# Kernel tuning notes

Measured on AMD Instinct MI355X. Metric: run time of the kernel, lower is better.

Reference implementation:

```python
import jax, jax.numpy as jnp
import numpy as np
import math

B, C, H, W, S = 8, 512, 64, 64, 4


def setup_inputs() -> dict:
    key = jax.random.key(0)
    ks = jax.random.split(key, 7)
    s = 1.0 / math.sqrt(C)  # ~ torch Linear init scale
    x = jax.random.normal(ks[0], (B, C, H, W), jnp.float32)
    Wq = jax.random.uniform(ks[1], (C, C), jnp.float32, -s, s)
    bq = jax.random.uniform(ks[2], (C,), jnp.float32, -s, s)
    Wk = jax.random.uniform(ks[3], (C, C), jnp.float32, -s, s)
    bk = jax.random.uniform(ks[4], (C,), jnp.float32, -s, s)
    Wv = jax.random.uniform(ks[5], (C, C), jnp.float32, -s, s)
    bv = jax.random.uniform(ks[6], (C,), jnp.float32, -s, s)
    return {"x": x, "Wq": Wq, "bq": bq, "Wk": Wk, "bk": bk, "Wv": Wv, "bv": bv}


def reference(x, Wq, bq, Wk, bk, Wv, bv):
    # x: (B, C, H, W). Faithful to the torch module's output, but expressed
    # in the algebraically-equivalent efficient form: the repeat_interleaved
    # attention matrix A is block-constant, so out = repeat(A_m @ Vsum).
    b, c, h, w = x.shape
    nb = (h // S) * (w // S)  # number of SxS spatial blocks
    hw = h * w
    ss = S * S

    # Block means in unfold order (bh, bw): (B, nb, C)
    x_avg = x.reshape(b, c, h // S, S, w // S, S).mean(axis=(3, 5))
    x_avg = x_avg.reshape(b, c, nb).transpose(0, 2, 1)

    Q = x_avg @ Wq.T + bq  # (B, nb, C)
    K = x_avg @ Wk.T + bk  # (B, nb, C)
    A = jax.nn.softmax(jnp.einsum('bnc,bmc->bnm', Q, K) / jnp.sqrt(jnp.float32(c)), axis=-1)

    # V over flat row-major pixels: (B, HW, C)
    x_flat = x.reshape(b, c, hw).transpose(0, 2, 1)
    V = x_flat @ Wv.T + bv

    # repeat_interleave on dim=2 means column group j of A sums V rows
    # [j*ss, (j+1)*ss) in FLAT pixel order (not spatial blocks) - faithful.
    Vsum = V.reshape(b, hw // ss, ss, c).sum(axis=2)  # (B, nb, C)
    out_small = jnp.einsum('bnm,bmc->bnc', A, Vsum)   # (B, nb, C)
    # repeat_interleave on dim=1: each block row broadcast to ss flat pixels
    out_flat = jnp.repeat(out_small, ss, axis=1)      # (B, HW, C)
    return out_flat.transpose(0, 2, 1).reshape(b, c, h, w)
```

## Files before the change

### kernel.cpp

```cpp
#include <hip/hip_runtime.h>

typedef __attribute__((ext_vector_type(8))) short short8;
typedef __attribute__((ext_vector_type(4))) float f32x4;

__device__ __forceinline__ unsigned short f2bf(float f) {
    union { float f; unsigned int i; } v; v.f = f;
    unsigned int x = v.i;
    return (unsigned short)((x + 0x7FFFu + ((x >> 16) & 1u)) >> 16);
}
__device__ __forceinline__ f32x4 mfma16(short8 a, short8 b, f32x4 c) {
    return __builtin_amdgcn_mfma_f32_16x16x32_bf16(a, b, c, 0, 0, 0);
}

__global__ void __launch_bounds__(256, 4)
prep_kernel(const float* __restrict__ x,
            const float* __restrict__ Wq,
            const float* __restrict__ Wk,
            const float* __restrict__ Wv,
            unsigned short* __restrict__ xavg,
            unsigned short* __restrict__ xsum,
            unsigned short* __restrict__ Wb)
{
    const int blk = blockIdx.x;
    const int t = threadIdx.x;
    if (blk >= 512) {
        const int f = (blk - 512) * 512 + t;
        const int m = f >> 16;
        const int o = f & 65535;
        const float4* s4 = (const float4*)((m == 0) ? Wq : (m == 1) ? Wk : Wv);
        float4 a = s4[o];
        float4 b = s4[o + 256];
        ushort4* d4 = (ushort4*)(Wb + (size_t)m * 262144);
        d4[o]       = make_ushort4(f2bf(a.x), f2bf(a.y), f2bf(a.z), f2bf(a.w));
        d4[o + 256] = make_ushort4(f2bf(b.x), f2bf(b.y), f2bf(b.z), f2bf(b.w));
        return;
    }

    const int b    = blk >> 6;
    const int rem  = blk & 63;
    const int cg   = rem >> 1;
    const int half = rem & 1;
    const int c0   = cg * 16;

    __shared__ float part[4][512];
    __shared__ unsigned short xsT[16][128];
    __shared__ unsigned short xaT[16][128];

    for (int cg4 = 0; cg4 < 4; ++cg4) {
        float4 a0, a1, b0, b1, c0v, c1, d0, d1;
        {
            const float* base = x + ((size_t)(b * 512 + c0 + cg4 * 4) * 4096) + half * 2048;
            const float4* p0 = (const float4*)(base);
            const float4* p1 = (const float4*)(base + 4096);
            const float4* p2 = (const float4*)(base + 8192);
            const float4* p3 = (const float4*)(base + 12288);
            a0 = p0[t]; a1 = p0[t + 256];
            b0 = p1[t]; b1 = p1[t + 256];
            c0v = p2[t]; c1 = p2[t + 256];
            d0 = p3[t]; d1 = p3[t + 256];
        }
        part[0][t]       = a0.x + a0.y + a0.z + a0.w;
        part[0][t + 256] = a1.x + a1.y + a1.z + a1.w;
        part[1][t]       = b0.x + b0.y + b0.z + b0.w;
        part[1][t + 256] = b1.x + b1.y + b1.z + b1.w;
        part[2][t]       = c0v.x + c0v.y + c0v.z + c0v.w;
        part[2][t + 256] = c1.x + c1.y + c1.z + c1.w;
        part[3][t]       = d0.x + d0.y + d0.z + d0.w;
        part[3][t + 256] = d1.x + d1.y + d1.z + d1.w;
        __syncthreads();

        if (t < 128) {
            const int g = t;
#pragma unroll
            for (int ci = 0; ci < 4; ++ci) {
                float4 q = *(const float4*)&part[ci][4 * g];
                xsT[cg4 * 4 + ci][g] = f2bf(q.x + q.y + q.z + q.w);
            }
        } else {
            const int n = t - 128;
            const int bh = n >> 4, bw = n & 15;
#pragma unroll
            for (int ci = 0; ci < 4; ++ci) {
                float m = (part[ci][(bh * 4 + 0) * 16 + bw] + part[ci][(bh * 4 + 1) * 16 + bw] +
                           part[ci][(bh * 4 + 2) * 16 + bw] + part[ci][(bh * 4 + 3) * 16 + bw]) * 0.0625f;
                xaT[cg4 * 4 + ci][n] = f2bf(m);
            }
        }
        __syncthreads();
    }

    {
        const int g = t >> 1, chunk = t & 1;
        const size_t rowbase = ((size_t)(b * 256) + half * 128 + g) * 512 + c0 + chunk * 8;
        short8 vs, va;
#pragma unroll
        for (int j = 0; j < 8; ++j) {
            vs[j] = (short)xsT[chunk * 8 + j][g];
            va[j] = (short)xaT[chunk * 8 + j][g];
        }
        *(short8*)(xsum + rowbase) = vs;
        *(short8*)(xavg + rowbase) = va;
    }
}

__global__ void __launch_bounds__(256, 3)
proj_gemm(const unsigned short* __restrict__ xavg,
          const unsigned short* __restrict__ xsum,
          const unsigned short* __restrict__ Wb,
          const float* __restrict__ bq,
          const float* __restrict__ bk,
          const float* __restrict__ bv,
          unsigned short* __restrict__ QK,
          unsigned short* __restrict__ VsT)
{
    const int blk = blockIdx.x;
    const int lane = threadIdx.x & 63, quad = lane >> 4, r16 = lane & 15;
    const int w = threadIdx.x >> 6;

    if (blk < 512) {
        const int wave = blk * 4 + w;
        const int mt = wave >> 5;
        const int nt = wave & 31;
        const unsigned short* xp0 = xavg + (size_t)(mt * 32 + r16) * 512 + quad * 8;
        const unsigned short* xp1 = xp0 + 16 * 512;
        const unsigned short* wp0 = Wb + (size_t)(nt * 32 + r16) * 512 + quad * 8;
        const unsigned short* wp1 = wp0 + 16 * 512;

        f32x4 a00 = {0,0,0,0}, a01 = a00, a10 = a00, a11 = a00;
#pragma unroll 4
        for (int k = 0; k < 512; k += 32) {
            short8 qa0 = *(const short8*)(xp0 + k);
            short8 qa1 = *(const short8*)(xp1 + k);
            short8 b0 = *(const short8*)(wp0 + k);
            short8 b1 = *(const short8*)(wp1 + k);
            a00 = mfma16(qa0, b0, a00); a01 = mfma16(qa0, b1, a01);
            a10 = mfma16(qa1, b0, a10); a11 = mfma16(qa1, b1, a11);
        }
        const int row0 = mt * 32 + quad * 4;
        f32x4 accs0[2] = {a00, a01};
        f32x4 accs1[2] = {a10, a11};
#pragma unroll
        for (int j = 0; j < 2; ++j) {
            const int c = nt * 32 + j * 16 + r16;
            const float bias = (c < 512) ? bq[c] : bk[c - 512];
#pragma unroll
            for (int r = 0; r < 4; ++r) {
                QK[(size_t)(row0 + r) * 1024 + c]      = f2bf(accs0[j][r] + bias);
                QK[(size_t)(row0 + 16 + r) * 1024 + c] = f2bf(accs1[j][r] + bias);
            }
        }
    } else {
        const int vblk = blk - 512;
        const int b = vblk >> 5;
        const int wib = (vblk & 31) * 4 + w;
        const int mt2 = wib >> 4;
        const int nt = wib & 15;
        const unsigned short* xp0 = xsum + (size_t)b * 131072 + (size_t)(mt2 * 32 + r16) * 512 + quad * 8;
        const unsigned short* xp1 = xp0 + 16 * 512;
        const unsigned short* wp0 = Wb + 524288 + (size_t)(nt * 32 + r16) * 512 + quad * 8;
        const unsigned short* wp1 = wp0 + 16 * 512;

        f32x4 a00 = {0,0,0,0}, a01 = a00, a10 = a00, a11 = a00;
#pragma unroll 4
        for (int k = 0; k < 512; k += 32) {
            short8 qa0 = *(const short8*)(xp0 + k);
            short8 qa1 = *(const short8*)(xp1 + k);
            short8 b0 = *(const short8*)(wp0 + k);
            short8 b1 = *(const short8*)(wp1 + k);
            a00 = mfma16(qa0, b0, a00); a01 = mfma16(qa0, b1, a01);
            a10 = mfma16(qa1, b0, a10); a11 = mfma16(qa1, b1, a11);
        }
        unsigned short* vb = VsT + (size_t)b * 131072;
        const int m0 = mt2 * 32 + quad * 4;
        f32x4 accs0[2] = {a00, a01};
        f32x4 accs1[2] = {a10, a11};
#pragma unroll
        for (int j = 0; j < 2; ++j) {
            const int c = nt * 32 + j * 16 + r16;
            const float bias = 16.f * bv[c];
#pragma unroll
            for (int r = 0; r < 4; ++r) {
                vb[(size_t)c * 256 + m0 + r]      = f2bf(accs0[j][r] + bias);
                vb[(size_t)c * 256 + m0 + 16 + r] = f2bf(accs1[j][r] + bias);
            }
        }
    }
}

__global__ void __launch_bounds__(256, 2)
score_av(const unsigned short* __restrict__ QK,
         const unsigned short* __restrict__ VsT,
         float* __restrict__ out)
{
    __shared__ union {
        float S[16][257];
        float osT[128][17];
    } u;
    __shared__ __align__(16) unsigned short Abf[16][264];

    const int b = blockIdx.y;
    const int strip = blockIdx.x >> 2;
    const int cq = blockIdx.x & 3;
    const int w = threadIdx.x >> 6, lane = threadIdx.x & 63;
    const int quad = lane >> 4, r16 = lane & 15;

    {
        const unsigned short* qp = QK + (size_t)(b * 256 + strip * 16 + r16) * 1024 + quad * 8;
        const unsigned short* kp0 = QK + (size_t)(b * 256 + w * 64 + r16) * 1024 + 512 + quad * 8;
        const unsigned short* kp1 = kp0 + 16 * 1024;
        const unsigned short* kp2 = kp0 + 32 * 1024;
        const unsigned short* kp3 = kp0 + 48 * 1024;

        f32x4 a0 = {0,0,0,0}, a1 = a0, a2 = a0, a3 = a0;
#pragma unroll 4
        for (int k = 0; k < 512; k += 32) {
            short8 qa = *(const short8*)(qp + k);
            short8 b0 = *(const short8*)(kp0 + k);
            short8 b1 = *(const short8*)(kp1 + k);
            short8 b2 = *(const short8*)(kp2 + k);
            short8 b3 = *(const short8*)(kp3 + k);
            a0 = mfma16(qa, b0, a0); a1 = mfma16(qa, b1, a1);
            a2 = mfma16(qa, b2, a2); a3 = mfma16(qa, b3, a3);
        }
        f32x4 accs[4] = {a0, a1, a2, a3};
#pragma unroll
        for (int j = 0; j < 4; ++j) {
            const int col = w * 64 + j * 16 + r16;
#pragma unroll
            for (int r = 0; r < 4; ++r)
                u.S[quad * 4 + r][col] = accs[j][r];
        }
    }
    __syncthreads();

    {
        const int t = threadIdx.x;
        const int r = t >> 4, idx = t & 15;
        float v[16];
        float mx = -3.4e38f;
#pragma unroll
        for (int j = 0; j < 16; ++j) {
            v[j] = u.S[r][idx * 16 + j] * 0.044194173824159216f;
            mx = fmaxf(mx, v[j]);
        }
        mx = fmaxf(mx, __shfl_xor(mx, 1));
        mx = fmaxf(mx, __shfl_xor(mx, 2));
        mx = fmaxf(mx, __shfl_xor(mx, 4));
        mx = fmaxf(mx, __shfl_xor(mx, 8));
        float sum = 0.f;
#pragma unroll
        for (int j = 0; j < 16; ++j) { v[j] = __expf(v[j] - mx); sum += v[j]; }
        sum += __shfl_xor(sum, 1);
        sum += __shfl_xor(sum, 2);
        sum += __shfl_xor(sum, 4);
        sum += __shfl_xor(sum, 8);
        const float inv = 1.f / sum;
        unsigned short* ap = &Abf[r][idx * 16];
#pragma unroll
        for (int j = 0; j < 16; j += 4)
            *(ushort4*)(ap + j) = make_ushort4(f2bf(v[j] * inv), f2bf(v[j + 1] * inv),
                                               f2bf(v[j + 2] * inv), f2bf(v[j + 3] * inv));
    }
    __syncthreads();

    {
        f32x4 acc0 = {0,0,0,0}, acc1 = acc0;
        const unsigned short* vp0 = VsT + (size_t)b * 131072 +
                                    (size_t)(cq * 128 + w * 32 + r16) * 256 + quad * 8;
        const unsigned short* vp1 = vp0 + 16 * 256;
#pragma unroll
        for (int kk = 0; kk < 256; kk += 32) {
            short8 a = *(const short8*)(&Abf[r16][kk + quad * 8]);
            short8 b0 = *(const short8*)(vp0 + kk);
            short8 b1 = *(const short8*)(vp1 + kk);
            acc0 = mfma16(a, b0, acc0); acc1 = mfma16(a, b1, acc1);
        }
        __syncthreads();
        f32x4 accs[2] = {acc0, acc1};
#pragma unroll
        for (int i = 0; i < 2; ++i) {
            const int cl = w * 32 + i * 16 + r16;
#pragma unroll
            for (int r = 0; r < 4; ++r)
                u.osT[cl][quad * 4 + r] = accs[i][r];
        }
    }
    __syncthreads();

    {
        const int j = threadIdx.x & 63;
        float* obase = out + (size_t)(b * 512 + cq * 128) * 4096 + strip * 256 + j * 4;
#pragma unroll
        for (int it = 0; it < 32; ++it) {
            const int ch = it * 4 + w;
            const float v = u.osT[ch][j >> 2];
            *(float4*)(obase + (size_t)ch * 4096) = make_float4(v, v, v, v);
        }
    }
}

extern "C" void kernel_launch(void* const* d_in, const int* in_sizes, int n_in,
                              void* d_out, int out_size, void* d_ws, size_t ws_size,
                              hipStream_t stream) {
    const float* x  = (const float*)d_in[0];
    const float* Wq = (const float*)d_in[1];
    const float* bq = (const float*)d_in[2];
    const float* Wk = (const float*)d_in[3];
    const float* bk = (const float*)d_in[4];
    const float* Wv = (const float*)d_in[5];
    const float* bv = (const float*)d_in[6];
    float* out = (float*)d_out;

    unsigned short* Wb   = (unsigned short*)d_ws;
    unsigned short* xavg = Wb + 786432;
    unsigned short* xsum = xavg + 1048576;
    unsigned short* QK   = xsum + 1048576;
    unsigned short* VsT  = QK + 2097152;

    prep_kernel<<<896, 256, 0, stream>>>(x, Wq, Wk, Wv, xavg, xsum, Wb);
    proj_gemm<<<768, 256, 0, stream>>>(xavg, xsum, Wb, bq, bk, bv, QK, VsT);
    score_av<<<dim3(64, 8), 256, 0, stream>>>(QK, VsT, out);
}
```

Measured before the change: 172.0 us.

## Split score/softmax and AV-expand into separate kernels to remove redundant score recomputation

```diff
diff --git a/kernel.cpp b/kernel.cpp
--- a/kernel.cpp
+++ b/kernel.cpp
@@ -188,19 +188,11 @@
 }
 
 __global__ void __launch_bounds__(256, 2)
-score_av(const unsigned short* __restrict__ QK,
-         const unsigned short* __restrict__ VsT,
-         float* __restrict__ out)
+score_softmax(const unsigned short* __restrict__ QK,
+              unsigned short* __restrict__ Amat)
 {
-    __shared__ union {
-        float S[16][257];
-        float osT[128][17];
-    } u;
-    __shared__ __align__(16) unsigned short Abf[16][264];
-
-    const int b = blockIdx.y;
-    const int strip = blockIdx.x >> 2;
-    const int cq = blockIdx.x & 3;
+    __shared__ float S[16][257];
+    const int b = blockIdx.y, strip = blockIdx.x;
     const int w = threadIdx.x >> 6, lane = threadIdx.x & 63;
     const int quad = lane >> 4, r16 = lane & 15;
 
@@ -228,7 +220,7 @@
             const int col = w * 64 + j * 16 + r16;
 #pragma unroll
             for (int r = 0; r < 4; ++r)
-                u.S[quad * 4 + r][col] = accs[j][r];
+                S[quad * 4 + r][col] = accs[j][r];
         }
     }
     __syncthreads();
@@ -240,7 +232,7 @@
         float mx = -3.4e38f;
 #pragma unroll
         for (int j = 0; j < 16; ++j) {
-            v[j] = u.S[r][idx * 16 + j] * 0.044194173824159216f;
+            v[j] = S[r][idx * 16 + j] * 0.044194173824159216f;
             mx = fmaxf(mx, v[j]);
         }
         mx = fmaxf(mx, __shfl_xor(mx, 1));
@@ -255,45 +247,53 @@
         sum += __shfl_xor(sum, 4);
         sum += __shfl_xor(sum, 8);
         const float inv = 1.f / sum;
-        unsigned short* ap = &Abf[r][idx * 16];
+        unsigned short* ap = Amat + (size_t)b * 65536 + (size_t)(strip * 16 + r) * 256 + idx * 16;
 #pragma unroll
         for (int j = 0; j < 16; j += 4)
             *(ushort4*)(ap + j) = make_ushort4(f2bf(v[j] * inv), f2bf(v[j + 1] * inv),
                                                f2bf(v[j + 2] * inv), f2bf(v[j + 3] * inv));
     }
+}
+
+__global__ void __launch_bounds__(256, 4)
+av_expand(const unsigned short* __restrict__ Amat,
+          const unsigned short* __restrict__ VsT,
+          float* __restrict__ out)
+{
+    __shared__ float osT[64][17];
+    const int b = blockIdx.y;
+    const int sh = blockIdx.x >> 3;
+    const int cq = blockIdx.x & 7;
+    const int w = threadIdx.x >> 6, lane = threadIdx.x & 63;
+    const int quad = lane >> 4, r16 = lane & 15;
+
+    {
+        const unsigned short* ap = Amat + (size_t)b * 65536 + (size_t)(sh * 16 + r16) * 256 + quad * 8;
+        const unsigned short* vp = VsT + (size_t)b * 131072 +
+                                   (size_t)(cq * 64 + w * 16 + r16) * 256 + quad * 8;
+        f32x4 acc = {0.f, 0.f, 0.f, 0.f};
+#pragma unroll
+        for (int k = 0; k < 256; k += 32) {
+            short8 a0 = *(const short8*)(ap + k);
+            short8 b0 = *(const short8*)(vp + k);
+            acc = mfma16(a0, b0, acc);
+        }
+#pragma unroll
+        for (int r = 0; r < 4; ++r)
+            osT[w * 16 + r16][quad * 4 + r] = acc[r];
+    }
     __syncthreads();
 
     {
-        f32x4 acc0 = {0,0,0,0}, acc1 = acc0;
-        const unsigned short* vp0 = VsT + (size_t)b * 131072 +
-                                    (size_t)(cq * 128 + w * 32 + r16) * 256 + quad * 8;
-        const unsigned short* vp1 = vp0 + 16 * 256;
-#pragma unroll
-        for (int kk = 0; kk < 256; kk += 32) {
-            short8 a = *(const short8*)(&Abf[r16][kk + quad * 8]);
-            short8 b0 = *(const short8*)(vp0 + kk);
-            short8 b1 = *(const short8*)(vp1 + kk);
-            acc0 = mfma16(a, b0, acc0); acc1 = mfma16(a, b1, acc1);
-        }
-        __syncthreads();
-        f32x4 accs[2] = {acc0, acc1};
-#pragma unroll
-        for (int i = 0; i < 2; ++i) {
-            const int cl = w * 32 + i * 16 + r16;
-#pragma unroll
-            for (int r = 0; r < 4; ++r)
-                u.osT[cl][quad * 4 + r] = accs[i][r];
-        }
-    }
-    __syncthreads();
-
-    {
-        const int j = threadIdx.x & 63;
-        float* obase = out + (size_t)(b * 512 + cq * 128) * 4096 + strip * 256 + j * 4;
-#pragma unroll
-        for (int it = 0; it < 32; ++it) {
-            const int ch = it * 4 + w;
-            const float v = u.osT[ch][j >> 2];
+        const int t = threadIdx.x;
+        const int ch4 = t >> 6;
+        const int j = t & 63;
+        const int n = j >> 2;
+        float* obase = out + (size_t)(b * 512 + cq * 64) * 4096 + sh * 256 + j * 4;
+#pragma unroll
+        for (int it = 0; it < 16; ++it) {
+            const int ch = it * 4 + ch4;
+            const float v = osT[ch][n];
             *(float4*)(obase + (size_t)ch * 4096) = make_float4(v, v, v, v);
         }
     }
@@ -316,8 +316,10 @@
     unsigned short* xsum = xavg + 1048576;
     unsigned short* QK   = xsum + 1048576;
     unsigned short* VsT  = QK + 2097152;
+    unsigned short* Amat = VsT + 1048576;
 
     prep_kernel<<<896, 256, 0, stream>>>(x, Wq, Wk, Wv, xavg, xsum, Wb);
     proj_gemm<<<768, 256, 0, stream>>>(xavg, xsum, Wb, bq, bk, bv, QK, VsT);
-    score_av<<<dim3(64, 8), 256, 0, stream>>>(QK, VsT, out);
-}
+    score_softmax<<<dim3(16, 8), 256, 0, stream>>>(QK, Amat);
+    av_expand<<<dim3(128, 8), 256, 0, stream>>>(Amat, VsT, out);
+}
```

New measurement: 173.5 us. Within noise of the previous version (+0.9%).
